# Optimization experiments

Measured on AMD Instinct MI355X. Metric: run time of the kernel, lower is better.

## Reference

```python
import jax, jax.numpy as jnp
import numpy as np

B, L, D, N, K = 4, 4096, 1024, 64, 3
EPS = 1e-6

def setup_inputs() -> dict:
    key = jax.random.key(0)
    ks = jax.random.split(key, 24)
    f32 = jnp.float32
    inp = {
        'T': jax.random.normal(ks[0], (B, L, D), f32),
        'norm_scale': jnp.ones((D,), f32),
        'in_w': jax.random.normal(ks[1], (2 * D, D), f32) * (1.0 / np.sqrt(D)),
        'in_b': jnp.zeros((2 * D,), f32),
        'dw_w': jax.random.normal(ks[2], (D, 1, K), f32) * (1.0 / np.sqrt(K)),
        'dw_b': jnp.zeros((D,), f32),
        'pw_w': jax.random.normal(ks[3], (D, D), f32) * (1.0 / np.sqrt(D)),
        'pw_b': jnp.zeros((D,), f32),
        'f_win': jax.random.normal(ks[4], (N, D), f32) * (1.0 / np.sqrt(D)),
        'f_wout': jax.random.normal(ks[5], (D, N), f32) * (1.0 / np.sqrt(N)),
        'f_logA': jax.random.normal(ks[6], (N,), f32) * 0.02,
        'f_B': jax.random.normal(ks[7], (N,), f32) * 0.02,
        'f_C': jax.random.normal(ks[8], (N,), f32) * 0.02,
        'f_logdt': jnp.array(0.0, f32),
        'b_win': jax.random.normal(ks[9], (N, D), f32) * (1.0 / np.sqrt(D)),
        'b_wout': jax.random.normal(ks[10], (D, N), f32) * (1.0 / np.sqrt(N)),
        'b_logA': jax.random.normal(ks[11], (N,), f32) * 0.02,
        'b_B': jax.random.normal(ks[12], (N,), f32) * 0.02,
        'b_C': jax.random.normal(ks[13], (N,), f32) * 0.02,
        'b_logdt': jnp.array(0.0, f32),
        'out_w': jax.random.normal(ks[14], (D, D), f32) * (1.0 / np.sqrt(D)),
        'out_b': jnp.zeros((D,), f32),
    }
    return inp

def _ssm(x, win, wout, logA, Bp, Cp, logdt):
    # ZOH discretization of diagonal SSM
    dt = jnp.exp(logdt)
    A = -jnp.exp(logA)
    Abar = jnp.exp(A * dt)
    denom = jnp.where(jnp.abs(A) < EPS, jnp.ones_like(A), A)
    frac = jnp.where(jnp.abs(A) < EPS, dt, (Abar - 1.0) / denom)
    Bbar = frac * Bp
    u = jnp.einsum('bld,nd->bln', x, win)  # (B,L,N)
    h0 = jnp.zeros((x.shape[0], win.shape[0]), x.dtype)
    def step(h, ut):
        h = h * Abar + ut * Bbar
        return h, h * Cp
    _, ys = jax.lax.scan(step, h0, jnp.swapaxes(u, 0, 1))  # (L,B,N)
    y = jnp.swapaxes(ys, 0, 1)
    return jnp.einsum('bln,dn->bld', y, wout)

def reference(T, norm_scale, in_w, in_b, dw_w, dw_b, pw_w, pw_b,
              f_win, f_wout, f_logA, f_B, f_C, f_logdt,
              b_win, b_wout, b_logA, b_B, b_C, b_logdt,
              out_w, out_b):
    # RMSNorm
    rms = jnp.sqrt(jnp.mean(T * T, axis=-1, keepdims=True) + EPS)
    Tn = T / rms * norm_scale
    # in_linear -> chunk
    xz = Tn @ in_w.T + in_b
    x, z = jnp.split(xz, 2, axis=-1)
    gate = jax.nn.sigmoid(z)
    # depthwise-separable conv1d (NCH layout)
    xc = jnp.swapaxes(x, 1, 2)  # (B,D,L)
    xc = jax.lax.conv_general_dilated(
        xc, dw_w, window_strides=(1,), padding=[(K // 2, K // 2)],
        dimension_numbers=('NCH', 'OIH', 'NCH'), feature_group_count=D)
    xc = xc + dw_b[None, :, None]
    xc = jnp.einsum('bdl,ed->bel', xc, pw_w) + pw_b[None, :, None]
    x_conv = jnp.swapaxes(xc, 1, 2)  # (B,L,D)
    # bidirectional SSM
    y_f = _ssm(x_conv, f_win, f_wout, f_logA, f_B, f_C, f_logdt)
    y_b = _ssm(jnp.flip(x_conv, axis=1), b_win, b_wout, b_logA, b_B, b_C, b_logdt)
    y_b = jnp.flip(y_b, axis=1)
    y = (y_f + y_b) * gate
    y = y @ out_w.T + out_b
    return T + y
```

## Files before the change

kernel.cpp:

```cpp
#include <hip/hip_runtime.h>
#include <cstdint>


#define L_SEQ 4096
#define D_DIM 1024
#define B_SZ 4
#define M_TOK (B_SZ * L_SEQ)
#define CHUNKS 64
#define CLEN (L_SEQ / CHUNKS)

typedef short bf16x8 __attribute__((ext_vector_type(8)));
typedef float floatx4 __attribute__((ext_vector_type(4)));

__device__ inline unsigned short f2bf(float f) {
  union { float f; unsigned int u; } v; v.f = f;
  unsigned int r = v.u + 0x7FFFu + ((v.u >> 16) & 1u);
  return (unsigned short)(r >> 16);
}
__device__ inline float bf2f(unsigned short h) {
  union { unsigned int u; float f; } v; v.u = ((unsigned int)h) << 16;
  return v.f;
}

__device__ inline void load_lds16(const unsigned short* g, unsigned short* l) {
  __builtin_amdgcn_global_load_lds(
      (const __attribute__((address_space(1))) unsigned int*)g,
      (__attribute__((address_space(3))) unsigned int*)l, 16, 0, 0);
}

__global__ __launch_bounds__(256) void rmsnorm_kernel(
    const float* __restrict__ T, const float* __restrict__ scale,
    unsigned short* __restrict__ Tn) {
  int tok = blockIdx.x;
  int t = threadIdx.x;
  const float4* row = (const float4*)(T + (size_t)tok * D_DIM);
  float4 v = row[t];
  float ss = v.x*v.x + v.y*v.y + v.z*v.z + v.w*v.w;
  #pragma unroll
  for (int off = 32; off > 0; off >>= 1) ss += __shfl_down(ss, off);
  __shared__ float part[4];
  if ((t & 63) == 0) part[t >> 6] = ss;
  __syncthreads();
  float total = part[0] + part[1] + part[2] + part[3];
  float rinv = rsqrtf(total * (1.0f / D_DIM) + 1e-6f);
  const float4* sc4 = (const float4*)scale;
  float4 s = sc4[t];
  ushort4 o;
  o.x = f2bf(v.x * rinv * s.x); o.y = f2bf(v.y * rinv * s.y);
  o.z = f2bf(v.z * rinv * s.z); o.w = f2bf(v.w * rinv * s.w);
  ((ushort4*)(Tn + (size_t)tok * D_DIM))[t] = o;
}

__global__ __launch_bounds__(256) void f2bf_vec_kernel(
    const float* __restrict__ in, unsigned short* __restrict__ out, int n4) {
  int i = blockIdx.x * 256 + threadIdx.x;
  if (i < n4) {
    float4 v = ((const float4*)in)[i];
    ushort4 o; o.x = f2bf(v.x); o.y = f2bf(v.y); o.z = f2bf(v.z); o.w = f2bf(v.w);
    ((ushort4*)out)[i] = o;
  }
}

__global__ void prepack_kernel(
    const float* __restrict__ f_win, const float* __restrict__ b_win,
    const float* __restrict__ f_wout, const float* __restrict__ b_wout,
    unsigned short* __restrict__ Wu, unsigned short* __restrict__ Wy) {
  int i = blockIdx.x * blockDim.x + threadIdx.x;
  if (i < 128 * D_DIM) {
    int n = i >> 10, k = i & (D_DIM - 1);
    Wu[i] = f2bf((n < 64) ? f_win[n * D_DIM + k] : b_win[(n - 64) * D_DIM + k]);
    int d = i >> 7, kk = i & 127;
    Wy[i] = f2bf((kk < 64) ? f_wout[d * 64 + kk] : b_wout[d * 64 + (kk - 64)]);
  }
}

template<int MODE, typename OUT_T>
__global__ __launch_bounds__(256) void gemm_mfma_kernel(
    const unsigned short* __restrict__ A, const unsigned short* __restrict__ Bw,
    const float* __restrict__ bias, OUT_T* __restrict__ out,
    int M, int N, int Kt,
    const void* __restrict__ aux0, unsigned short* __restrict__ aux1) {
  __shared__ unsigned short As[2][128 * 32];
  __shared__ unsigned short Bs[2][128 * 32];
  int tid = threadIdx.x;
  int wave = tid >> 6, lane = tid & 63;
  int quad = lane >> 4, lrow = lane & 15;
  int bm = blockIdx.y * 128, bn = blockIdx.x * 128;
  int wm = (wave & 1) * 64, wn = (wave >> 1) * 64;

  int r0 = tid >> 2;
  int c8 = (tid & 3) * 8;
  const unsigned short* Ag0 = A  + (size_t)(bm + r0) * Kt + c8;
  const unsigned short* Ag1 = A  + (size_t)(bm + 64 + r0) * Kt + c8;
  const unsigned short* Bg0 = Bw + (size_t)(bn + r0) * Kt + c8;
  const unsigned short* Bg1 = Bw + (size_t)(bn + 64 + r0) * Kt + c8;
  int woff = wave * 512;

  floatx4 acc[4][4] = {};
  int nt = Kt >> 5;

  load_lds16(Ag0, &As[0][0] + woff);
  load_lds16(Ag1, &As[0][0] + 2048 + woff);
  load_lds16(Bg0, &Bs[0][0] + woff);
  load_lds16(Bg1, &Bs[0][0] + 2048 + woff);
  __syncthreads();

  int cur = 0;
  for (int t = 0; t < nt; ++t) {
    if (t + 1 < nt) {
      int k0 = (t + 1) << 5;
      int nb = cur ^ 1;
      load_lds16(Ag0 + k0, &As[nb][0] + woff);
      load_lds16(Ag1 + k0, &As[nb][0] + 2048 + woff);
      load_lds16(Bg0 + k0, &Bs[nb][0] + woff);
      load_lds16(Bg1 + k0, &Bs[nb][0] + 2048 + woff);
    }
    {
      const unsigned short* Ab = &As[cur][0];
      const unsigned short* Bb = &Bs[cur][0];
      bf16x8 af[4], bfr[4];
      #pragma unroll
      for (int mi = 0; mi < 4; ++mi)
        af[mi] = *(const bf16x8*)(Ab + (wm + mi * 16 + lrow) * 32 + quad * 8);
      #pragma unroll
      for (int ni = 0; ni < 4; ++ni)
        bfr[ni] = *(const bf16x8*)(Bb + (wn + ni * 16 + lrow) * 32 + quad * 8);
      __builtin_amdgcn_s_setprio(1);
      #pragma unroll
      for (int mi = 0; mi < 4; ++mi)
        #pragma unroll
        for (int ni = 0; ni < 4; ++ni)
          acc[mi][ni] = __builtin_amdgcn_mfma_f32_16x16x32_bf16(
              af[mi], bfr[ni], acc[mi][ni], 0, 0, 0);
      __builtin_amdgcn_s_setprio(0);
    }
    if (t + 1 < nt) {
      __syncthreads();
      cur ^= 1;
    }
  }

  #pragma unroll
  for (int mi = 0; mi < 4; ++mi) {
    #pragma unroll
    for (int ni = 0; ni < 4; ++ni) {
      #pragma unroll
      for (int r = 0; r < 4; ++r) {
        int m = bm + wm + mi * 16 + quad * 4 + r;
        int n = bn + wn + ni * 16 + lrow;
        float v = acc[mi][ni][r];
        if (MODE == 0) {
          if (bias) v += bias[n];
          if (sizeof(OUT_T) == 2) out[(size_t)m * N + n] = (OUT_T)f2bf(v);
          else                    out[(size_t)m * N + n] = (OUT_T)v;
        } else if (MODE == 1) {
          if (bias) v += bias[n];
          if (n < D_DIM) ((unsigned short*)out)[(size_t)m * D_DIM + n] = f2bf(v);
          else aux1[(size_t)m * D_DIM + (n - D_DIM)] = f2bf(1.0f / (1.0f + expf(-v)));
        } else if (MODE == 2) {
          v *= bf2f(((const unsigned short*)aux0)[(size_t)m * N + n]);
          ((unsigned short*)out)[(size_t)m * N + n] = f2bf(v);
        } else {
          if (bias) v += bias[n];
          v += ((const float*)aux0)[(size_t)m * N + n];
          ((float*)out)[(size_t)m * N + n] = v;
        }
      }
    }
  }
}

__global__ __launch_bounds__(256) void dwconv_kernel(
    const unsigned short* __restrict__ x, const float* __restrict__ w,
    const float* __restrict__ b, unsigned short* __restrict__ out) {
  size_t i8 = (size_t)blockIdx.x * 256 + threadIdx.x;
  int d8 = (int)(i8 & (D_DIM / 8 - 1));
  size_t tok = i8 >> 7;
  int l = (int)(tok & (L_SEQ - 1));
  int d0 = d8 * 8;
  size_t base = tok * D_DIM + d0;
  bf16x8 cur = *(const bf16x8*)(x + base);
  float acc[8];
  #pragma unroll
  for (int j = 0; j < 8; ++j) {
    int d = d0 + j;
    acc[j] = b[d] + w[d * 3 + 1] * bf2f((unsigned short)cur[j]);
  }
  if (l > 0) {
    bf16x8 prv = *(const bf16x8*)(x + base - D_DIM);
    #pragma unroll
    for (int j = 0; j < 8; ++j) acc[j] += w[(d0 + j) * 3 + 0] * bf2f((unsigned short)prv[j]);
  }
  if (l < L_SEQ - 1) {
    bf16x8 nxt = *(const bf16x8*)(x + base + D_DIM);
    #pragma unroll
    for (int j = 0; j < 8; ++j) acc[j] += w[(d0 + j) * 3 + 2] * bf2f((unsigned short)nxt[j]);
  }
  bf16x8 o;
  #pragma unroll
  for (int j = 0; j < 8; ++j) o[j] = (short)f2bf(acc[j]);
  *(bf16x8*)(out + base) = o;
}

__device__ inline void ssm_params(
    int col,
    const float* f_logA, const float* f_B, const float* f_C, const float* f_logdt,
    const float* b_logA, const float* b_B, const float* b_C, const float* b_logdt,
    float& Abar, float& Bbar, float& Cc, float& Aa, float& dt) {
  int dir = col >> 6, n = col & 63;
  const float* logA  = dir ? b_logA  : f_logA;
  const float* Bp    = dir ? b_B     : f_B;
  const float* Cp    = dir ? b_C     : f_C;
  const float* logdt = dir ? b_logdt : f_logdt;
  dt = expf(logdt[0]);
  Aa = -expf(logA[n]);
  Abar = expf(Aa * dt);
  float frac = (fabsf(Aa) < 1e-6f) ? dt : (Abar - 1.0f) / Aa;
  Bbar = frac * Bp[n];
  Cc = Cp[n];
}

__global__ __launch_bounds__(128) void scan_s1_kernel(
    const float* __restrict__ u, float* __restrict__ states,
    const float* __restrict__ f_logA, const float* __restrict__ f_B,
    const float* __restrict__ f_C, const float* __restrict__ f_logdt,
    const float* __restrict__ b_logA, const float* __restrict__ b_B,
    const float* __restrict__ b_C, const float* __restrict__ b_logdt) {
  int col = threadIdx.x;
  int chunk = blockIdx.x, b = blockIdx.y;
  float Abar, Bbar, Cc, Aa, dt;
  ssm_params(col, f_logA, f_B, f_C, f_logdt, b_logA, b_B, b_C, b_logdt,
             Abar, Bbar, Cc, Aa, dt);
  size_t base = ((size_t)b * L_SEQ + (size_t)chunk * CLEN) * 128 + col;
  float h = 0.0f;
  if (col < 64) {
    for (int i0 = 0; i0 < CLEN; i0 += 8) {
      float uv[8];
      #pragma unroll
      for (int j = 0; j < 8; ++j) uv[j] = u[base + (size_t)(i0 + j) * 128];
      #pragma unroll
      for (int j = 0; j < 8; ++j) h = h * Abar + uv[j] * Bbar;
    }
  } else {
    for (int i0 = CLEN - 1; i0 >= 0; i0 -= 8) {
      float uv[8];
      #pragma unroll
      for (int j = 0; j < 8; ++j) uv[j] = u[base + (size_t)(i0 - j) * 128];
      #pragma unroll
      for (int j = 0; j < 8; ++j) h = h * Abar + uv[j] * Bbar;
    }
  }
  states[((size_t)b * CHUNKS + chunk) * 128 + col] = h;
}

__global__ __launch_bounds__(512) void scan_s2_kernel(
    const float* __restrict__ states, float* __restrict__ carries,
    const float* __restrict__ f_logA, const float* __restrict__ f_B,
    const float* __restrict__ f_C, const float* __restrict__ f_logdt,
    const float* __restrict__ b_logA, const float* __restrict__ b_B,
    const float* __restrict__ b_C, const float* __restrict__ b_logdt) {
  int tid = threadIdx.x;
  int b = tid >> 7, col = tid & 127;
  float Abar, Bbar, Cc, Aa, dt;
  ssm_params(col, f_logA, f_B, f_C, f_logdt, b_logA, b_B, b_C, b_logdt,
             Abar, Bbar, Cc, Aa, dt);
  float Ac = expf(Aa * dt * (float)CLEN);
  size_t sb = (size_t)b * CHUNKS * 128 + col;
  float cur = 0.0f;
  if (col < 64) {
    for (int c = 0; c < CHUNKS; ++c) {
      carries[sb + (size_t)c * 128] = cur;
      cur = cur * Ac + states[sb + (size_t)c * 128];
    }
  } else {
    for (int c = CHUNKS - 1; c >= 0; --c) {
      carries[sb + (size_t)c * 128] = cur;
      cur = cur * Ac + states[sb + (size_t)c * 128];
    }
  }
}

__global__ __launch_bounds__(128) void scan_s3_kernel(
    const float* __restrict__ u, const float* __restrict__ carries,
    unsigned short* __restrict__ y,
    const float* __restrict__ f_logA, const float* __restrict__ f_B,
    const float* __restrict__ f_C, const float* __restrict__ f_logdt,
    const float* __restrict__ b_logA, const float* __restrict__ b_B,
    const float* __restrict__ b_C, const float* __restrict__ b_logdt) {
  int col = threadIdx.x;
  int chunk = blockIdx.x, b = blockIdx.y;
  float Abar, Bbar, Cc, Aa, dt;
  ssm_params(col, f_logA, f_B, f_C, f_logdt, b_logA, b_B, b_C, b_logdt,
             Abar, Bbar, Cc, Aa, dt);
  size_t base = ((size_t)b * L_SEQ + (size_t)chunk * CLEN) * 128 + col;
  float h = carries[((size_t)b * CHUNKS + chunk) * 128 + col];
  if (col < 64) {
    for (int i0 = 0; i0 < CLEN; i0 += 8) {
      float uv[8];
      #pragma unroll
      for (int j = 0; j < 8; ++j) uv[j] = u[base + (size_t)(i0 + j) * 128];
      #pragma unroll
      for (int j = 0; j < 8; ++j) {
        h = h * Abar + uv[j] * Bbar;
        y[base + (size_t)(i0 + j) * 128] = f2bf(h * Cc);
      }
    }
  } else {
    for (int i0 = CLEN - 1; i0 >= 0; i0 -= 8) {
      float uv[8];
      #pragma unroll
      for (int j = 0; j < 8; ++j) uv[j] = u[base + (size_t)(i0 - j) * 128];
      #pragma unroll
      for (int j = 0; j < 8; ++j) {
        h = h * Abar + uv[j] * Bbar;
        y[base + (size_t)(i0 - j) * 128] = f2bf(h * Cc);
      }
    }
  }
}

extern "C" void kernel_launch(void* const* d_in, const int* in_sizes, int n_in,
                              void* d_out, int out_size, void* d_ws, size_t ws_size,
                              hipStream_t stream) {
  const float* T         = (const float*)d_in[0];
  const float* norm_scale= (const float*)d_in[1];
  const float* in_w      = (const float*)d_in[2];
  const float* in_b      = (const float*)d_in[3];
  const float* dw_w      = (const float*)d_in[4];
  const float* dw_b      = (const float*)d_in[5];
  const float* pw_w      = (const float*)d_in[6];
  const float* pw_b      = (const float*)d_in[7];
  const float* f_win     = (const float*)d_in[8];
  const float* f_wout    = (const float*)d_in[9];
  const float* f_logA    = (const float*)d_in[10];
  const float* f_B       = (const float*)d_in[11];
  const float* f_C       = (const float*)d_in[12];
  const float* f_logdt   = (const float*)d_in[13];
  const float* b_win     = (const float*)d_in[14];
  const float* b_wout    = (const float*)d_in[15];
  const float* b_logA    = (const float*)d_in[16];
  const float* b_B       = (const float*)d_in[17];
  const float* b_C       = (const float*)d_in[18];
  const float* b_logdt   = (const float*)d_in[19];
  const float* out_w     = (const float*)d_in[20];
  const float* out_b     = (const float*)d_in[21];
  float* out = (float*)d_out;

  char* ws = (char*)d_ws;
  const size_t MD = (size_t)M_TOK * D_DIM;
  unsigned short* gate  = (unsigned short*)ws;              ws += MD * 2;
  unsigned short* bufA  = (unsigned short*)ws;              ws += MD * 2;
  unsigned short* bufB  = (unsigned short*)ws;              ws += MD * 2;
  float*          u     = (float*)ws;                       ws += (size_t)M_TOK * 128 * 4;
  unsigned short* ybuf  = (unsigned short*)ws;              ws += (size_t)M_TOK * 128 * 2;
  unsigned short* w_in  = (unsigned short*)ws;              ws += (size_t)2 * D_DIM * D_DIM * 2;
  unsigned short* w_pw  = (unsigned short*)ws;              ws += (size_t)D_DIM * D_DIM * 2;
  unsigned short* w_out = (unsigned short*)ws;              ws += (size_t)D_DIM * D_DIM * 2;
  unsigned short* Wu    = (unsigned short*)ws;              ws += (size_t)128 * D_DIM * 2;
  unsigned short* Wy    = (unsigned short*)ws;              ws += (size_t)128 * D_DIM * 2;
  float*          states= (float*)ws;                       ws += (size_t)B_SZ * CHUNKS * 128 * 4;
  float*          carries=(float*)ws;

  f2bf_vec_kernel<<<(2 * D_DIM * D_DIM / 4 + 255) / 256, 256, 0, stream>>>(in_w, w_in, 2 * D_DIM * D_DIM / 4);
  f2bf_vec_kernel<<<(D_DIM * D_DIM / 4 + 255) / 256, 256, 0, stream>>>(pw_w, w_pw, D_DIM * D_DIM / 4);
  f2bf_vec_kernel<<<(D_DIM * D_DIM / 4 + 255) / 256, 256, 0, stream>>>(out_w, w_out, D_DIM * D_DIM / 4);
  prepack_kernel<<<(128 * D_DIM) / 256, 256, 0, stream>>>(f_win, b_win, f_wout, b_wout, Wu, Wy);
  rmsnorm_kernel<<<M_TOK, 256, 0, stream>>>(T, norm_scale, bufA);
  {
    dim3 g((2 * D_DIM) / 128, M_TOK / 128);
    gemm_mfma_kernel<1, unsigned short><<<g, 256, 0, stream>>>(
        bufA, w_in, in_b, bufB, M_TOK, 2 * D_DIM, D_DIM, nullptr, gate);
  }
  dwconv_kernel<<<(MD / 8) / 256, 256, 0, stream>>>(bufB, dw_w, dw_b, bufA);
  {
    dim3 g(D_DIM / 128, M_TOK / 128);
    gemm_mfma_kernel<0, unsigned short><<<g, 256, 0, stream>>>(
        bufA, w_pw, pw_b, bufB, M_TOK, D_DIM, D_DIM, nullptr, nullptr);
  }
  {
    dim3 g(1, M_TOK / 128);
    gemm_mfma_kernel<0, float><<<g, 256, 0, stream>>>(
        bufB, Wu, nullptr, u, M_TOK, 128, D_DIM, nullptr, nullptr);
  }
  {
    dim3 g1(CHUNKS, B_SZ);
    scan_s1_kernel<<<g1, 128, 0, stream>>>(u, states, f_logA, f_B, f_C, f_logdt,
                                           b_logA, b_B, b_C, b_logdt);
    scan_s2_kernel<<<1, 512, 0, stream>>>(states, carries, f_logA, f_B, f_C, f_logdt,
                                          b_logA, b_B, b_C, b_logdt);
    scan_s3_kernel<<<g1, 128, 0, stream>>>(u, carries, ybuf, f_logA, f_B, f_C, f_logdt,
                                           b_logA, b_B, b_C, b_logdt);
  }
  {
    dim3 g(D_DIM / 128, M_TOK / 128);
    gemm_mfma_kernel<2, unsigned short><<<g, 256, 0, stream>>>(
        ybuf, Wy, nullptr, bufA, M_TOK, D_DIM, 128, gate, nullptr);
  }
  {
    dim3 g(D_DIM / 128, M_TOK / 128);
    gemm_mfma_kernel<3, float><<<g, 256, 0, stream>>>(
        bufA, w_out, out_b, out, M_TOK, D_DIM, D_DIM, T, nullptr);
  }
}
```

Before: 622.0 us.

## Add 256x256-tile pipelined MFMA GEMM and use it for large projections

Adds a new GEMM kernel that works on 256x256 output tiles with 512 threads and a 64-wide K step. It double-buffers LDS with direct global-to-LDS loads, uses a rotated LDS layout to avoid bank conflicts, and swizzles the workgroup order. The intent is more data reuse per tile and better overlap of loads with MFMA work across the four large GEMMs. In exchange it uses far more LDS and registers per block and launches fewer workgroups, which may reduce occupancy.

```diff
diff --git a/kernel.cpp b/kernel.cpp
--- a/kernel.cpp
+++ b/kernel.cpp
@@ -71,6 +71,140 @@
     Wu[i] = f2bf((n < 64) ? f_win[n * D_DIM + k] : b_win[(n - 64) * D_DIM + k]);
     int d = i >> 7, kk = i & 127;
     Wy[i] = f2bf((kk < 64) ? f_wout[d * 64 + kk] : b_wout[d * 64 + (kk - 64)]);
+  }
+}
+
+template<int MODE, typename OUT_T>
+__global__ __launch_bounds__(512, 2) void gemm256_kernel(
+    const unsigned short* __restrict__ A, const unsigned short* __restrict__ Bw,
+    const float* __restrict__ bias, OUT_T* __restrict__ out,
+    int M, int N, int Kt,
+    const void* __restrict__ aux0, unsigned short* __restrict__ aux1) {
+  __shared__ __align__(16) unsigned short As2[2][256 * 64];
+  __shared__ __align__(16) unsigned short Bs2[2][256 * 64];
+  const int tid = threadIdx.x;
+  const int w = tid >> 6, lane = tid & 63;
+  const int quad = lane >> 4, lrow = lane & 15;
+  const int wm = w >> 2, wn = w & 3;
+
+  const int nx = N >> 8;
+  const int nwg = nx * (M >> 8);
+  int obid = blockIdx.y * nx + blockIdx.x;
+  int swz = (nwg & 7) ? obid : ((obid & 7) * (nwg >> 3) + (obid >> 3));
+  const int bm = (swz / nx) << 8;
+  const int bn = (swz % nx) << 8;
+
+  const int lr = lane >> 3, ls = lane & 7;
+  const int laneOff = lr * Kt + (((ls - lr) & 7) << 3);
+  const unsigned short* Asrc = A + (size_t)bm * Kt + laneOff;
+  const unsigned short* Bsrc = Bw + (size_t)bn * Kt + laneOff;
+
+  floatx4 acc[8][4] = {};
+
+  const int nkt = Kt >> 6;
+  const int nIter = nkt >> 1;
+
+  auto stageA = [&](int buf, int h, int kt) {
+    int t0 = h * 64 + w * 8;
+    int t1 = 128 + h * 64 + w * 8;
+    load_lds16(Asrc + (size_t)t0 * Kt + kt * 64, &As2[buf][t0 * 64]);
+    load_lds16(Asrc + (size_t)t1 * Kt + kt * 64, &As2[buf][t1 * 64]);
+  };
+  auto stageB = [&](int buf, int kt) {
+    #pragma unroll
+    for (int j = 0; j < 4; ++j) {
+      int t0 = j * 64 + w * 8;
+      load_lds16(Bsrc + (size_t)t0 * Kt + kt * 64, &Bs2[buf][t0 * 64]);
+    }
+  };
+  auto fragAddr = [&](int r, int ks) {
+    return (r << 6) + ((((ks << 2) + quad + r) & 7) << 3);
+  };
+
+  stageA(0, 0, 0); stageB(0, 0); stageA(0, 1, 0);
+  stageA(1, 0, 1); stageB(1, 1);
+  asm volatile("s_waitcnt vmcnt(6)" ::: "memory");
+  __builtin_amdgcn_s_barrier();
+
+  const int rA0 = wm * 128 + lrow;
+  const int rB0 = wn * 64 + lrow;
+
+  for (int i = 0; i < nIter; ++i) {
+    const int t2 = 2 * i + 2, t3 = 2 * i + 3;
+    const bool s2 = t2 < nkt, s3 = t3 < nkt;
+    bf16x8 af[4], bfr[4];
+
+    #pragma unroll
+    for (int half = 0; half < 2; ++half) {
+      const unsigned short* Ab = As2[half];
+      const unsigned short* Bb = Bs2[half];
+      #pragma unroll
+      for (int ph = 0; ph < 4; ++ph) {
+        const int h = ph & 1, ks = ph >> 1;
+        if (h == 0) {
+          #pragma unroll
+          for (int ni = 0; ni < 4; ++ni)
+            bfr[ni] = *(const bf16x8*)(Bb + fragAddr(rB0 + ni * 16, ks));
+        }
+        #pragma unroll
+        for (int mi = 0; mi < 4; ++mi)
+          af[mi] = *(const bf16x8*)(Ab + fragAddr(rA0 + h * 64 + mi * 16, ks));
+        if (half == 0) {
+          if (ph == 0) stageA(1, 1, 2 * i + 1);
+          if (ph == 3 && s2) { stageA(0, 0, t2); stageB(0, t2); }
+        } else {
+          if (ph == 0 && s2) stageA(0, 1, t2);
+          if (ph == 3 && s3) { stageA(1, 0, t3); stageB(1, t3); }
+        }
+        if (ph == 3) {
+          if ((half == 0) ? s2 : s3)
+            asm volatile("s_waitcnt vmcnt(6)" ::: "memory");
+          else
+            asm volatile("s_waitcnt vmcnt(0)" ::: "memory");
+        }
+        __builtin_amdgcn_s_barrier();
+        asm volatile("s_waitcnt lgkmcnt(0)" ::: "memory");
+        __builtin_amdgcn_sched_barrier(0);
+        __builtin_amdgcn_s_setprio(1);
+        #pragma unroll
+        for (int mi = 0; mi < 4; ++mi)
+          #pragma unroll
+          for (int ni = 0; ni < 4; ++ni)
+            acc[h * 4 + mi][ni] = __builtin_amdgcn_mfma_f32_16x16x32_bf16(
+                af[mi], bfr[ni], acc[h * 4 + mi][ni], 0, 0, 0);
+        __builtin_amdgcn_s_setprio(0);
+        __builtin_amdgcn_s_barrier();
+      }
+    }
+  }
+
+  #pragma unroll
+  for (int mi8 = 0; mi8 < 8; ++mi8) {
+    #pragma unroll
+    for (int ni = 0; ni < 4; ++ni) {
+      #pragma unroll
+      for (int r = 0; r < 4; ++r) {
+        int m = bm + wm * 128 + mi8 * 16 + quad * 4 + r;
+        int n = bn + wn * 64 + ni * 16 + lrow;
+        float v = acc[mi8][ni][r];
+        if (MODE == 0) {
+          if (bias) v += bias[n];
+          if (sizeof(OUT_T) == 2) out[(size_t)m * N + n] = (OUT_T)f2bf(v);
+          else                    out[(size_t)m * N + n] = (OUT_T)v;
+        } else if (MODE == 1) {
+          if (bias) v += bias[n];
+          if (n < D_DIM) ((unsigned short*)out)[(size_t)m * D_DIM + n] = f2bf(v);
+          else aux1[(size_t)m * D_DIM + (n - D_DIM)] = f2bf(1.0f / (1.0f + expf(-v)));
+        } else if (MODE == 2) {
+          v *= bf2f(((const unsigned short*)aux0)[(size_t)m * N + n]);
+          ((unsigned short*)out)[(size_t)m * N + n] = f2bf(v);
+        } else {
+          if (bias) v += bias[n];
+          v += ((const float*)aux0)[(size_t)m * N + n];
+          ((float*)out)[(size_t)m * N + n] = v;
+        }
+      }
+    }
   }
 }
 
@@ -367,14 +501,14 @@
   prepack_kernel<<<(128 * D_DIM) / 256, 256, 0, stream>>>(f_win, b_win, f_wout, b_wout, Wu, Wy);
   rmsnorm_kernel<<<M_TOK, 256, 0, stream>>>(T, norm_scale, bufA);
   {
-    dim3 g((2 * D_DIM) / 128, M_TOK / 128);
-    gemm_mfma_kernel<1, unsigned short><<<g, 256, 0, stream>>>(
+    dim3 g((2 * D_DIM) / 256, M_TOK / 256);
+    gemm256_kernel<1, unsigned short><<<g, 512, 0, stream>>>(
         bufA, w_in, in_b, bufB, M_TOK, 2 * D_DIM, D_DIM, nullptr, gate);
   }
   dwconv_kernel<<<(MD / 8) / 256, 256, 0, stream>>>(bufB, dw_w, dw_b, bufA);
   {
-    dim3 g(D_DIM / 128, M_TOK / 128);
-    gemm_mfma_kernel<0, unsigned short><<<g, 256, 0, stream>>>(
+    dim3 g(D_DIM / 256, M_TOK / 256);
+    gemm256_kernel<0, unsigned short><<<g, 512, 0, stream>>>(
         bufA, w_pw, pw_b, bufB, M_TOK, D_DIM, D_DIM, nullptr, nullptr);
   }
   {
@@ -392,13 +526,13 @@
                                            b_logA, b_B, b_C, b_logdt);
   }
   {
-    dim3 g(D_DIM / 128, M_TOK / 128);
-    gemm_mfma_kernel<2, unsigned short><<<g, 256, 0, stream>>>(
+    dim3 g(D_DIM / 256, M_TOK / 256);
+    gemm256_kernel<2, unsigned short><<<g, 512, 0, stream>>>(
         ybuf, Wy, nullptr, bufA, M_TOK, D_DIM, 128, gate, nullptr);
   }
   {
-    dim3 g(D_DIM / 128, M_TOK / 128);
-    gemm_mfma_kernel<3, float><<<g, 256, 0, stream>>>(
+    dim3 g(D_DIM / 256, M_TOK / 256);
+    gemm256_kernel<3, float><<<g, 512, 0, stream>>>(
         bufA, w_out, out_b, out, M_TOK, D_DIM, D_DIM, T, nullptr);
   }
 }
```

Result: slower. 743.9 us (+19.6%).

## Fold pointwise conv weights into SSM input projection, remove pw GEMM

Applied to the files above, without the earlier changes.

Precomputes Wf = win·pw_w and a bias cb = win·pw_b, so the SSM input projection reads the depthwise-conv output directly. This removes the full M×D×D pointwise GEMM and its bf16 intermediate buffer. It also adds an XCD-aware workgroup swizzle to the GEMM tile mapping and switches the sigmoid to fast __expf. The weight fusion runs every call as a small fp32 kernel, and rounding differs slightly because the fused weights are quantized to bf16 once.

```diff
diff --git a/kernel.cpp b/kernel.cpp
--- a/kernel.cpp
+++ b/kernel.cpp
@@ -61,17 +61,47 @@
   }
 }
 
-__global__ void prepack_kernel(
-    const float* __restrict__ f_win, const float* __restrict__ b_win,
+__global__ void prepack_wy_kernel(
     const float* __restrict__ f_wout, const float* __restrict__ b_wout,
-    unsigned short* __restrict__ Wu, unsigned short* __restrict__ Wy) {
+    unsigned short* __restrict__ Wy) {
   int i = blockIdx.x * blockDim.x + threadIdx.x;
   if (i < 128 * D_DIM) {
-    int n = i >> 10, k = i & (D_DIM - 1);
-    Wu[i] = f2bf((n < 64) ? f_win[n * D_DIM + k] : b_win[(n - 64) * D_DIM + k]);
     int d = i >> 7, kk = i & 127;
     Wy[i] = f2bf((kk < 64) ? f_wout[d * 64 + kk] : b_wout[d * 64 + (kk - 64)]);
   }
+}
+
+__global__ __launch_bounds__(256) void fuse_wu_kernel(
+    const float* __restrict__ f_win, const float* __restrict__ b_win,
+    const float* __restrict__ pw_w, unsigned short* __restrict__ Wf) {
+  int d = blockIdx.x * 256 + threadIdx.x;
+  int n0 = blockIdx.y * 8;
+  const float* w0 = (n0 < 64) ? (f_win + (size_t)n0 * D_DIM)
+                              : (b_win + (size_t)(n0 - 64) * D_DIM);
+  float acc[8] = {};
+  #pragma unroll 4
+  for (int e = 0; e < D_DIM; ++e) {
+    float p = pw_w[(size_t)e * D_DIM + d];
+    #pragma unroll
+    for (int j = 0; j < 8; ++j)
+      acc[j] = fmaf(p, w0[(size_t)j * D_DIM + e], acc[j]);
+  }
+  #pragma unroll
+  for (int j = 0; j < 8; ++j)
+    Wf[(size_t)(n0 + j) * D_DIM + d] = f2bf(acc[j]);
+}
+
+__global__ __launch_bounds__(64) void cbias_kernel(
+    const float* __restrict__ f_win, const float* __restrict__ b_win,
+    const float* __restrict__ pw_b, float* __restrict__ cb) {
+  int n = blockIdx.x, t = threadIdx.x;
+  const float* wrow = (n < 64) ? (f_win + (size_t)n * D_DIM)
+                               : (b_win + (size_t)(n - 64) * D_DIM);
+  float s = 0.0f;
+  for (int e = t; e < D_DIM; e += 64) s += wrow[e] * pw_b[e];
+  #pragma unroll
+  for (int off = 32; off > 0; off >>= 1) s += __shfl_down(s, off);
+  if (t == 0) cb[n] = s;
 }
 
 template<int MODE, typename OUT_T>
@@ -85,7 +115,11 @@
   int tid = threadIdx.x;
   int wave = tid >> 6, lane = tid & 63;
   int quad = lane >> 4, lrow = lane & 15;
-  int bm = blockIdx.y * 128, bn = blockIdx.x * 128;
+  int nx = N >> 7;
+  int nwg = nx * (M >> 7);
+  int obid = blockIdx.y * nx + blockIdx.x;
+  int swz = (nwg & 7) ? obid : ((obid & 7) * (nwg >> 3) + (obid >> 3));
+  int bm = (swz / nx) << 7, bn = (swz % nx) << 7;
   int wm = (wave & 1) * 64, wn = (wave >> 1) * 64;
 
   int r0 = tid >> 2;
@@ -156,7 +190,7 @@
         } else if (MODE == 1) {
           if (bias) v += bias[n];
           if (n < D_DIM) ((unsigned short*)out)[(size_t)m * D_DIM + n] = f2bf(v);
-          else aux1[(size_t)m * D_DIM + (n - D_DIM)] = f2bf(1.0f / (1.0f + expf(-v)));
+          else aux1[(size_t)m * D_DIM + (n - D_DIM)] = f2bf(1.0f / (1.0f + __expf(-v)));
         } else if (MODE == 2) {
           v *= bf2f(((const unsigned short*)aux0)[(size_t)m * N + n]);
           ((unsigned short*)out)[(size_t)m * N + n] = f2bf(v);
@@ -354,17 +388,21 @@
   float*          u     = (float*)ws;                       ws += (size_t)M_TOK * 128 * 4;
   unsigned short* ybuf  = (unsigned short*)ws;              ws += (size_t)M_TOK * 128 * 2;
   unsigned short* w_in  = (unsigned short*)ws;              ws += (size_t)2 * D_DIM * D_DIM * 2;
-  unsigned short* w_pw  = (unsigned short*)ws;              ws += (size_t)D_DIM * D_DIM * 2;
   unsigned short* w_out = (unsigned short*)ws;              ws += (size_t)D_DIM * D_DIM * 2;
-  unsigned short* Wu    = (unsigned short*)ws;              ws += (size_t)128 * D_DIM * 2;
+  unsigned short* Wf    = (unsigned short*)ws;              ws += (size_t)128 * D_DIM * 2;
   unsigned short* Wy    = (unsigned short*)ws;              ws += (size_t)128 * D_DIM * 2;
+  float*          cb    = (float*)ws;                       ws += 128 * 4;
   float*          states= (float*)ws;                       ws += (size_t)B_SZ * CHUNKS * 128 * 4;
   float*          carries=(float*)ws;
 
   f2bf_vec_kernel<<<(2 * D_DIM * D_DIM / 4 + 255) / 256, 256, 0, stream>>>(in_w, w_in, 2 * D_DIM * D_DIM / 4);
-  f2bf_vec_kernel<<<(D_DIM * D_DIM / 4 + 255) / 256, 256, 0, stream>>>(pw_w, w_pw, D_DIM * D_DIM / 4);
   f2bf_vec_kernel<<<(D_DIM * D_DIM / 4 + 255) / 256, 256, 0, stream>>>(out_w, w_out, D_DIM * D_DIM / 4);
-  prepack_kernel<<<(128 * D_DIM) / 256, 256, 0, stream>>>(f_win, b_win, f_wout, b_wout, Wu, Wy);
+  prepack_wy_kernel<<<(128 * D_DIM) / 256, 256, 0, stream>>>(f_wout, b_wout, Wy);
+  {
+    dim3 g(D_DIM / 256, 16);
+    fuse_wu_kernel<<<g, 256, 0, stream>>>(f_win, b_win, pw_w, Wf);
+  }
+  cbias_kernel<<<128, 64, 0, stream>>>(f_win, b_win, pw_b, cb);
   rmsnorm_kernel<<<M_TOK, 256, 0, stream>>>(T, norm_scale, bufA);
   {
     dim3 g((2 * D_DIM) / 128, M_TOK / 128);
@@ -373,14 +411,9 @@
   }
   dwconv_kernel<<<(MD / 8) / 256, 256, 0, stream>>>(bufB, dw_w, dw_b, bufA);
   {
-    dim3 g(D_DIM / 128, M_TOK / 128);
-    gemm_mfma_kernel<0, unsigned short><<<g, 256, 0, stream>>>(
-        bufA, w_pw, pw_b, bufB, M_TOK, D_DIM, D_DIM, nullptr, nullptr);
-  }
-  {
     dim3 g(1, M_TOK / 128);
     gemm_mfma_kernel<0, float><<<g, 256, 0, stream>>>(
-        bufB, Wu, nullptr, u, M_TOK, 128, D_DIM, nullptr, nullptr);
+        bufA, Wf, cb, u, M_TOK, 128, D_DIM, nullptr, nullptr);
   }
   {
     dim3 g1(CHUNKS, B_SZ);
```

Result: slower. 678.7 us (+9.1%).
